# Kernel optimization log

Measured on AMD Instinct MI355X. Metric: run time of the kernel, lower is better.

The kernel has to match this reference:

```python
import jax, jax.numpy as jnp
import numpy as np

N_NODES = 100000
N_EDGES = 1000000
N_GRAPHS = 512
IN_DIM = 3
HID = 64


def setup_inputs() -> dict:
    key = jax.random.key(0)
    ks = jax.random.split(key, 7)
    x = jax.random.normal(ks[0], (N_NODES, IN_DIM), dtype=jnp.float32)
    edge_index = jax.random.randint(ks[1], (2, N_EDGES), 0, N_NODES, dtype=jnp.int64)
    batch = jnp.sort(jax.random.randint(ks[2], (N_NODES,), 0, N_GRAPHS, dtype=jnp.int64))
    # Glorot-ish init for GCNConv linear weights (PyG uses glorot), zero bias.
    W1 = jax.random.normal(ks[3], (IN_DIM, HID), dtype=jnp.float32) / np.float32(np.sqrt(IN_DIM))
    b1 = jnp.zeros((HID,), dtype=jnp.float32)
    W2 = jax.random.normal(ks[4], (HID, HID), dtype=jnp.float32) / np.float32(np.sqrt(HID))
    b2 = jnp.zeros((HID,), dtype=jnp.float32)
    return {"x": x, "W1": W1, "b1": b1, "W2": W2, "b2": b2,
            "edge_index": edge_index, "batch": batch}


def reference(x, W1, b1, W2, b2, edge_index, batch):
    n = x.shape[0]
    loop = jnp.arange(n)
    # GCNConv adds self-loops, then symmetric normalization D^-1/2 (A+I) D^-1/2
    src = jnp.concatenate([edge_index[0], loop])  # [E+N]
    dst = jnp.concatenate([edge_index[1], loop])  # [E+N]
    deg = jax.ops.segment_sum(jnp.ones(dst.shape[0], x.dtype), dst, num_segments=n)
    dinv = jnp.where(deg > 0, jax.lax.rsqrt(deg), 0.0)
    norm = dinv[src] * dinv[dst]  # [E+N]

    def gcn_conv(h, W, b):
        hw = h @ W                       # [N, out] linear first (PyG order)
        msg = hw[src] * norm[:, None]    # gather + scale, [E+N, out]
        agg = jax.ops.segment_sum(msg, dst, num_segments=n)  # scatter-add
        return agg + b

    h = jax.nn.relu(gcn_conv(x, W1, b1))
    h = jax.nn.relu(gcn_conv(h, W2, b2))

    # global_mean_pool over the batch vector
    sums = jax.ops.segment_sum(h, batch, num_segments=N_GRAPHS)          # [G, HID]
    counts = jax.ops.segment_sum(jnp.ones(n, h.dtype), batch, num_segments=N_GRAPHS)
    return sums / jnp.maximum(counts, 1.0)[:, None]
```

## Files before the change

### kernel.cpp

```cpp
#include <hip/hip_runtime.h>

#define HID 64
#define N_GRAPHS_C 512
#define BSHIFT 8
#define NBUCK_MAX 512
#define CAP 3264
#define EPB 4096

typedef unsigned short u16;
typedef unsigned int u32;
typedef unsigned long long u64;

__device__ __forceinline__ float bf2f(u16 u) {
    union { u32 i; float f; } v; v.i = ((u32)u) << 16; return v.f;
}
__device__ __forceinline__ u16 f2bf(float f) {
    union { float f; u32 i; } v; v.f = f;
    u32 x = v.i;
    return (u16)((x + 0x7fffu + ((x >> 16) & 1u)) >> 16);
}


__global__ void bin_pairs(const int* __restrict__ src, const int* __restrict__ dst,
                          int* __restrict__ gcursor, u32* __restrict__ pairs,
                          int nE, int nbuck) {
    __shared__ int lh[NBUCK_MAX];
    __shared__ int lbase[NBUCK_MAX];
    int t = threadIdx.x;
    lh[t] = 0; lh[t + 256] = 0;
    __syncthreads();
    int base = blockIdx.x * EPB;
    u32 pk[16]; int rj[16], bj[16];
    #pragma unroll
    for (int j = 0; j < 16; ++j) {
        int e = base + j * 256 + t;
        if (e < nE) {
            int s = src[e], d = dst[e];
            bj[j] = d >> BSHIFT;
            pk[j] = ((u32)(d & 255) << 17) | (u32)s;
            rj[j] = atomicAdd(&lh[bj[j]], 1);
        } else {
            bj[j] = -1;
        }
    }
    __syncthreads();
    for (int b = t; b < nbuck; b += 256)
        lbase[b] = (lh[b] > 0) ? atomicAdd(&gcursor[b], lh[b]) : 0;
    __syncthreads();
    #pragma unroll
    for (int j = 0; j < 16; ++j) {
        if (bj[j] >= 0) {
            int pos = bj[j] * CAP + lbase[bj[j]] + rj[j];
            pairs[pos] = pk[j];
        }
    }
}

__global__ void build_csr(const u32* __restrict__ pairs, const int* __restrict__ gcursor,
                          int* __restrict__ csr_src, int2* __restrict__ off2,
                          float* __restrict__ dinv, const float* __restrict__ x,
                          float4* __restrict__ xs, u16* __restrict__ A16, int n) {
    __shared__ int hist[256];
    __shared__ int tmp[256];
    int t = threadIdx.x;
    int b = blockIdx.x;
    int pbeg = b * CAP;
    int pend = pbeg + gcursor[b];
    hist[t] = 0;
    if (b == 0 && t < 32) ((u32*)(A16 + (size_t)n * HID))[t] = 0;
    __syncthreads();
    for (int i = pbeg + t; i < pend; i += 256)
        atomicAdd(&hist[pairs[i] >> 17], 1);
    __syncthreads();
    int v = hist[t];
    tmp[t] = v;
    __syncthreads();
    for (int d = 1; d < 256; d <<= 1) {
        int add = (t >= d) ? tmp[t - d] : 0;
        __syncthreads();
        tmp[t] += add;
        __syncthreads();
    }
    int e = pbeg + tmp[t] - v;
    int node = (b << BSHIFT) + t;
    if (node < n) {
        float dv = rsqrtf((float)(v + 1));
        off2[node] = make_int2(e, e + v);
        dinv[node] = dv;
        xs[node] = make_float4(x[3*node]*dv, x[3*node+1]*dv, x[3*node+2]*dv, dv);
    }
    hist[t] = e;
    __syncthreads();
    for (int i = pbeg + t; i < pend; i += 256) {
        u32 p = pairs[i];
        int pos = atomicAdd(&hist[p >> 17], 1);
        csr_src[pos] = (int)(p & 0x1FFFFu);
    }
}


__global__ void agg3(const float4* __restrict__ xs, const int* __restrict__ csr_src,
                     const int2* __restrict__ off2, float4* __restrict__ agg4, int n) {
    int node = blockIdx.x * blockDim.x + threadIdx.x;
    if (node >= n) return;
    int2 be = off2[node];
    int beg = be.x, end = be.y;
    float4 self = xs[node];
    float a0 = 0.f, a1 = 0.f, a2 = 0.f;
    for (int k = beg; k < end; k += 8) {
        int e1 = end - 1;
        int idx[8];
        float4 v[8];
        #pragma unroll
        for (int j = 0; j < 8; ++j) idx[j] = csr_src[min(k + j, e1)];
        #pragma unroll
        for (int j = 0; j < 8; ++j) v[j] = xs[idx[j]];
        #pragma unroll
        for (int j = 0; j < 8; ++j) {
            if (k + j < end) { a0 += v[j].x; a1 += v[j].y; a2 += v[j].z; }
        }
    }
    agg4[node] = make_float4(a0 + self.x, a1 + self.y, a2 + self.z, self.w);
}


#define MM2_NODES 32
__global__ void mm2f(const float4* __restrict__ agg4, const float* __restrict__ W1,
                     const float* __restrict__ b1, const float* __restrict__ W2,
                     u16* __restrict__ A16, int n) {
    __shared__ float w[HID * HID];
    __shared__ float h[MM2_NODES * HID];
    __shared__ float dd[MM2_NODES];
    int t = threadIdx.x;
    for (int i = t; i < HID * HID; i += 256) w[i] = W2[i];
    int base = blockIdx.x * MM2_NODES;
    for (int i = t; i < MM2_NODES * HID; i += 256) {
        int node = base + (i >> 6);
        int f = i & 63;
        float hv = 0.0f;
        if (node < n) {
            float4 a = agg4[node];
            float v = (a.x * W1[f] + a.y * W1[HID + f] + a.z * W1[2 * HID + f]) * a.w + b1[f];
            hv = v > 0.0f ? v : 0.0f;
            if (f == 0) dd[i >> 6] = a.w;
        }
        h[i] = hv;
    }
    __syncthreads();
    int f = t & 63, g = t >> 6;
    float acc[8];
    #pragma unroll
    for (int j = 0; j < 8; ++j) acc[j] = 0.0f;
    #pragma unroll 4
    for (int k = 0; k < HID; ++k) {
        float wk = w[k * HID + f];
        #pragma unroll
        for (int j = 0; j < 8; ++j) acc[j] += h[(g * 8 + j) * HID + k] * wk;
    }
    #pragma unroll
    for (int j = 0; j < 8; ++j) {
        int node = base + g * 8 + j;
        if (node < n) A16[(size_t)node * HID + f] = f2bf(acc[j] * dd[g * 8 + j]);
    }
}


__global__ void gather_nodes(const u16* __restrict__ A16, const float* __restrict__ dinv,
                             const int* __restrict__ csr_src, const int2* __restrict__ off2,
                             const float* __restrict__ bias,
                             u16* __restrict__ H16, int n) {
    int t = threadIdx.x;
    int waveq = t >> 4;
    int m = t & 15;
    int qbase = t & 48;
    int node = blockIdx.x * 16 + waveq;
    if (node >= n) return;
    int2 be = off2[node];
    int beg = be.x, end = be.y;
    u64 selfrow = *(const u64*)(A16 + ((size_t)node << 6) + (m << 2));
    u32 slo = (u32)selfrow, shi = (u32)(selfrow >> 32);
    float acc0 = bf2f((u16)(slo & 0xffffu));
    float acc1 = bf2f((u16)(slo >> 16));
    float acc2 = bf2f((u16)(shi & 0xffffu));
    float acc3 = bf2f((u16)(shi >> 16));
    const char* Ab = (const char*)A16;
    u32 laneoff = (u32)(m << 3);
    for (int k = beg; k < end; k += 16) {
        int nIdx = end - k;
        int myIdx = (m < nIdx) ? csr_src[k + m] : n;
        #pragma unroll
        for (int j0 = 0; j0 < 16; j0 += 8) {
            int ss[8]; u64 rows[8];
            #pragma unroll
            for (int j = 0; j < 8; ++j)
                ss[j] = __shfl(myIdx, qbase + j0 + j, 64);
            #pragma unroll
            for (int j = 0; j < 8; ++j)
                rows[j] = *(const u64*)(Ab + (((u32)ss[j] << 7) | laneoff));
            #pragma unroll
            for (int j = 0; j < 8; ++j) {
                u32 lo = (u32)rows[j], hi = (u32)(rows[j] >> 32);
                acc0 += bf2f((u16)(lo & 0xffffu));
                acc1 += bf2f((u16)(lo >> 16));
                acc2 += bf2f((u16)(hi & 0xffffu));
                acc3 += bf2f((u16)(hi >> 16));
            }
        }
    }
    float ddv = dinv[node];
    float4 bb = *(const float4*)(bias + (m << 2));
    float v0 = fmaxf(acc0 * ddv + bb.x, 0.0f);
    float v1 = fmaxf(acc1 * ddv + bb.y, 0.0f);
    float v2 = fmaxf(acc2 * ddv + bb.z, 0.0f);
    float v3 = fmaxf(acc3 * ddv + bb.w, 0.0f);
    u64 outp = (u64)f2bf(v0) | ((u64)f2bf(v1) << 16)
             | ((u64)f2bf(v2) << 32) | ((u64)f2bf(v3) << 48);
    *(u64*)(H16 + ((size_t)node << 6) + (m << 2)) = outp;
}


__device__ __forceinline__ int lower_bound(const int* __restrict__ a, int n, int key) {
    int lo = 0, hi = n;
    while (lo < hi) {
        int mid = (lo + hi) >> 1;
        if (a[mid] < key) lo = mid + 1; else hi = mid;
    }
    return lo;
}

__global__ void graph_ranges(const int* __restrict__ batch, int* __restrict__ gstart,
                             int n, int nGraphs) {
    for (int g = threadIdx.x; g <= nGraphs; g += blockDim.x)
        gstart[g] = lower_bound(batch, n, g);
}


__global__ void pool_graph(const u16* __restrict__ H16, const int* __restrict__ gstart,
                           float* __restrict__ out, int n) {
    int g = blockIdx.x;
    int t = threadIdx.x;
    int lo = gstart[g];
    int hi = gstart[g + 1];
    int cntN = hi - lo;
    int sid = t >> 4;
    int m = t & 15;
    float a0 = 0.f, a1 = 0.f, a2 = 0.f, a3 = 0.f;
    int i = lo + sid;
    for (; i + 16 < hi; i += 32) {
        u64 r0 = *(const u64*)(H16 + ((size_t)i << 6) + (m << 2));
        u64 r1 = *(const u64*)(H16 + ((size_t)(i + 16) << 6) + (m << 2));
        u32 l0 = (u32)r0, h0 = (u32)(r0 >> 32);
        u32 l1 = (u32)r1, h1 = (u32)(r1 >> 32);
        a0 += bf2f((u16)(l0 & 0xffffu)) + bf2f((u16)(l1 & 0xffffu));
        a1 += bf2f((u16)(l0 >> 16))     + bf2f((u16)(l1 >> 16));
        a2 += bf2f((u16)(h0 & 0xffffu)) + bf2f((u16)(h1 & 0xffffu));
        a3 += bf2f((u16)(h0 >> 16))     + bf2f((u16)(h1 >> 16));
    }
    if (i < hi) {
        u64 r0 = *(const u64*)(H16 + ((size_t)i << 6) + (m << 2));
        u32 l0 = (u32)r0, h0 = (u32)(r0 >> 32);
        a0 += bf2f((u16)(l0 & 0xffffu));
        a1 += bf2f((u16)(l0 >> 16));
        a2 += bf2f((u16)(h0 & 0xffffu));
        a3 += bf2f((u16)(h0 >> 16));
    }
    a0 += __shfl_xor(a0, 16, 64); a0 += __shfl_xor(a0, 32, 64);
    a1 += __shfl_xor(a1, 16, 64); a1 += __shfl_xor(a1, 32, 64);
    a2 += __shfl_xor(a2, 16, 64); a2 += __shfl_xor(a2, 32, 64);
    a3 += __shfl_xor(a3, 16, 64); a3 += __shfl_xor(a3, 32, 64);
    __shared__ float smf[4 * HID];
    int wave = t >> 6, lane = t & 63;
    if (lane < 16) {
        smf[wave * HID + 4 * lane + 0] = a0;
        smf[wave * HID + 4 * lane + 1] = a1;
        smf[wave * HID + 4 * lane + 2] = a2;
        smf[wave * HID + 4 * lane + 3] = a3;
    }
    __syncthreads();
    if (t < HID) {
        float s = smf[t] + smf[HID + t] + smf[2 * HID + t] + smf[3 * HID + t];
        out[(size_t)g * HID + t] = s / fmaxf((float)cntN, 1.0f);
    }
}


extern "C" void kernel_launch(void* const* d_in, const int* in_sizes, int n_in,
                              void* d_out, int out_size, void* d_ws, size_t ws_size,
                              hipStream_t stream) {
    const float* x  = (const float*)d_in[0];
    const float* W1 = (const float*)d_in[1];
    const float* b1 = (const float*)d_in[2];
    const float* W2 = (const float*)d_in[3];
    const float* b2 = (const float*)d_in[4];
    const int*   ei = (const int*)d_in[5];
    const int*   batch = (const int*)d_in[6];

    const int n  = in_sizes[0] / 3;
    const int nE = in_sizes[5] / 2;
    const int* src = ei;
    const int* dst = ei + nE;
    const int nbuck = (n + ((1 << BSHIFT) - 1)) >> BSHIFT;
    const int nGraphs = out_size / HID;

    char* p = (char*)d_ws;
    int*    gcursor = (int*)p;                p += 2048;
    int*    gstart  = (int*)p;                p += 4096;
    int*    csr_src = (int*)p;                p += (size_t)nbuck * CAP * 4;
    int2*   off2    = (int2*)p;               p += (size_t)n * 8;
    float*  dinv    = (float*)p;              p += (size_t)n * 4;
    float4* xs      = (float4*)p;             p += (size_t)n * 16;
    float4* agg4    = (float4*)p;             p += (size_t)n * 16;
    u16*    A16     = (u16*)p;                p += (size_t)(n + 1) * HID * 2;
    u16*    H2      = (u16*)p;                p += (size_t)n * HID * 2;
    u32*    pairs   = (u32*)A16;

    const int BT = 256;
    const int gridNode = (n + BT - 1) / BT;
    const int gridE2   = (nE + EPB - 1) / EPB;
    const int gridMM2  = (n + MM2_NODES - 1) / MM2_NODES;
    const int gridGath = (n + 15) / 16;

    hipMemsetAsync(gcursor, 0, 2048, stream);
    bin_pairs<<<gridE2, BT, 0, stream>>>(src, dst, gcursor, pairs, nE, nbuck);
    build_csr<<<nbuck, BT, 0, stream>>>(pairs, gcursor, csr_src, off2, dinv, x, xs, A16, n);

    graph_ranges<<<1, 512, 0, stream>>>(batch, gstart, n, nGraphs);

    agg3<<<gridNode, BT, 0, stream>>>(xs, csr_src, off2, agg4, n);
    mm2f<<<gridMM2, BT, 0, stream>>>(agg4, W1, b1, W2, A16, n);

    gather_nodes<<<gridGath, BT, 0, stream>>>(A16, dinv, csr_src, off2, b2, H2, n);

    pool_graph<<<nGraphs, BT, 0, stream>>>(H2, gstart, (float*)d_out, n);
}
```

Before: 172.0 us.

## Fuse memset with graph-range prep, widen binning blocks, shrink gather unroll

Replaces the memset and the graph_ranges launch with a single prep kernel that zeroes the bucket cursors and computes graph start offsets, removing one launch and one memset. bin_pairs and build_csr now run with 512 threads per block, so bin_pairs keeps 8 edges per thread instead of 16 and build_csr guards its 256-wide scan and node work to the first 256 threads. The second-layer gather loop handles 8 neighbours per iteration instead of 16, which wastes fewer padded lanes on low-degree nodes but leaves fewer loads in flight per iteration. The zeroing in prep relies on nbuck being at most 512.

```diff
diff --git a/kernel.cpp b/kernel.cpp
--- a/kernel.cpp
+++ b/kernel.cpp
@@ -21,19 +21,37 @@
 }
 
 
+__device__ __forceinline__ int lower_bound(const int* __restrict__ a, int n, int key) {
+    int lo = 0, hi = n;
+    while (lo < hi) {
+        int mid = (lo + hi) >> 1;
+        if (a[mid] < key) lo = mid + 1; else hi = mid;
+    }
+    return lo;
+}
+
+__global__ void prep(int* __restrict__ gcursor, const int* __restrict__ batch,
+                     int* __restrict__ gstart, int n, int nGraphs) {
+    int t = threadIdx.x;
+    gcursor[t] = 0;
+    for (int g = t; g <= nGraphs; g += 512)
+        gstart[g] = lower_bound(batch, n, g);
+}
+
+
 __global__ void bin_pairs(const int* __restrict__ src, const int* __restrict__ dst,
                           int* __restrict__ gcursor, u32* __restrict__ pairs,
                           int nE, int nbuck) {
     __shared__ int lh[NBUCK_MAX];
     __shared__ int lbase[NBUCK_MAX];
     int t = threadIdx.x;
-    lh[t] = 0; lh[t + 256] = 0;
+    lh[t] = 0;
     __syncthreads();
     int base = blockIdx.x * EPB;
-    u32 pk[16]; int rj[16], bj[16];
+    u32 pk[8]; int rj[8], bj[8];
     #pragma unroll
-    for (int j = 0; j < 16; ++j) {
-        int e = base + j * 256 + t;
+    for (int j = 0; j < 8; ++j) {
+        int e = base + j * 512 + t;
         if (e < nE) {
             int s = src[e], d = dst[e];
             bj[j] = d >> BSHIFT;
@@ -44,11 +62,10 @@
         }
     }
     __syncthreads();
-    for (int b = t; b < nbuck; b += 256)
-        lbase[b] = (lh[b] > 0) ? atomicAdd(&gcursor[b], lh[b]) : 0;
+    if (t < nbuck) lbase[t] = (lh[t] > 0) ? atomicAdd(&gcursor[t], lh[t]) : 0;
     __syncthreads();
     #pragma unroll
-    for (int j = 0; j < 16; ++j) {
+    for (int j = 0; j < 8; ++j) {
         if (bj[j] >= 0) {
             int pos = bj[j] * CAP + lbase[bj[j]] + rj[j];
             pairs[pos] = pk[j];
@@ -66,32 +83,34 @@
     int b = blockIdx.x;
     int pbeg = b * CAP;
     int pend = pbeg + gcursor[b];
-    hist[t] = 0;
+    if (t < 256) hist[t] = 0;
     if (b == 0 && t < 32) ((u32*)(A16 + (size_t)n * HID))[t] = 0;
     __syncthreads();
-    for (int i = pbeg + t; i < pend; i += 256)
+    for (int i = pbeg + t; i < pend; i += 512)
         atomicAdd(&hist[pairs[i] >> 17], 1);
     __syncthreads();
-    int v = hist[t];
-    tmp[t] = v;
+    int v = 0;
+    if (t < 256) { v = hist[t]; tmp[t] = v; }
     __syncthreads();
     for (int d = 1; d < 256; d <<= 1) {
-        int add = (t >= d) ? tmp[t - d] : 0;
+        int add = (t >= d && t < 256) ? tmp[t - d] : 0;
         __syncthreads();
-        tmp[t] += add;
+        if (t < 256) tmp[t] += add;
         __syncthreads();
     }
-    int e = pbeg + tmp[t] - v;
-    int node = (b << BSHIFT) + t;
-    if (node < n) {
-        float dv = rsqrtf((float)(v + 1));
-        off2[node] = make_int2(e, e + v);
-        dinv[node] = dv;
-        xs[node] = make_float4(x[3*node]*dv, x[3*node+1]*dv, x[3*node+2]*dv, dv);
-    }
-    hist[t] = e;
-    __syncthreads();
-    for (int i = pbeg + t; i < pend; i += 256) {
+    if (t < 256) {
+        int e = pbeg + tmp[t] - v;
+        int node = (b << BSHIFT) + t;
+        if (node < n) {
+            float dv = rsqrtf((float)(v + 1));
+            off2[node] = make_int2(e, e + v);
+            dinv[node] = dv;
+            xs[node] = make_float4(x[3*node]*dv, x[3*node+1]*dv, x[3*node+2]*dv, dv);
+        }
+        hist[t] = e;
+    }
+    __syncthreads();
+    for (int i = pbeg + t; i < pend; i += 512) {
         u32 p = pairs[i];
         int pos = atomicAdd(&hist[p >> 17], 1);
         csr_src[pos] = (int)(p & 0x1FFFFu);
@@ -185,26 +204,23 @@
     float acc3 = bf2f((u16)(shi >> 16));
     const char* Ab = (const char*)A16;
     u32 laneoff = (u32)(m << 3);
-    for (int k = beg; k < end; k += 16) {
-        int nIdx = end - k;
-        int myIdx = (m < nIdx) ? csr_src[k + m] : n;
-        #pragma unroll
-        for (int j0 = 0; j0 < 16; j0 += 8) {
-            int ss[8]; u64 rows[8];
-            #pragma unroll
-            for (int j = 0; j < 8; ++j)
-                ss[j] = __shfl(myIdx, qbase + j0 + j, 64);
-            #pragma unroll
-            for (int j = 0; j < 8; ++j)
-                rows[j] = *(const u64*)(Ab + (((u32)ss[j] << 7) | laneoff));
-            #pragma unroll
-            for (int j = 0; j < 8; ++j) {
-                u32 lo = (u32)rows[j], hi = (u32)(rows[j] >> 32);
-                acc0 += bf2f((u16)(lo & 0xffffu));
-                acc1 += bf2f((u16)(lo >> 16));
-                acc2 += bf2f((u16)(hi & 0xffffu));
-                acc3 += bf2f((u16)(hi >> 16));
-            }
+    for (int k = beg; k < end; k += 8) {
+        int lim = min(end - k, 8);
+        int myIdx = (m < lim) ? csr_src[k + m] : n;
+        int ss[8]; u64 rows[8];
+        #pragma unroll
+        for (int j = 0; j < 8; ++j)
+            ss[j] = __shfl(myIdx, qbase + j, 64);
+        #pragma unroll
+        for (int j = 0; j < 8; ++j)
+            rows[j] = *(const u64*)(Ab + (((u32)ss[j] << 7) | laneoff));
+        #pragma unroll
+        for (int j = 0; j < 8; ++j) {
+            u32 lo = (u32)rows[j], hi = (u32)(rows[j] >> 32);
+            acc0 += bf2f((u16)(lo & 0xffffu));
+            acc1 += bf2f((u16)(lo >> 16));
+            acc2 += bf2f((u16)(hi & 0xffffu));
+            acc3 += bf2f((u16)(hi >> 16));
         }
     }
     float ddv = dinv[node];
@@ -216,22 +232,6 @@
     u64 outp = (u64)f2bf(v0) | ((u64)f2bf(v1) << 16)
              | ((u64)f2bf(v2) << 32) | ((u64)f2bf(v3) << 48);
     *(u64*)(H16 + ((size_t)node << 6) + (m << 2)) = outp;
-}
-
-
-__device__ __forceinline__ int lower_bound(const int* __restrict__ a, int n, int key) {
-    int lo = 0, hi = n;
-    while (lo < hi) {
-        int mid = (lo + hi) >> 1;
-        if (a[mid] < key) lo = mid + 1; else hi = mid;
-    }
-    return lo;
-}
-
-__global__ void graph_ranges(const int* __restrict__ batch, int* __restrict__ gstart,
-                             int n, int nGraphs) {
-    for (int g = threadIdx.x; g <= nGraphs; g += blockDim.x)
-        gstart[g] = lower_bound(batch, n, g);
 }
 
 
@@ -320,11 +320,9 @@
     const int gridMM2  = (n + MM2_NODES - 1) / MM2_NODES;
     const int gridGath = (n + 15) / 16;
 
-    hipMemsetAsync(gcursor, 0, 2048, stream);
-    bin_pairs<<<gridE2, BT, 0, stream>>>(src, dst, gcursor, pairs, nE, nbuck);
-    build_csr<<<nbuck, BT, 0, stream>>>(pairs, gcursor, csr_src, off2, dinv, x, xs, A16, n);
-
-    graph_ranges<<<1, 512, 0, stream>>>(batch, gstart, n, nGraphs);
+    prep<<<1, 512, 0, stream>>>(gcursor, batch, gstart, n, nGraphs);
+    bin_pairs<<<gridE2, 512, 0, stream>>>(src, dst, gcursor, pairs, nE, nbuck);
+    build_csr<<<nbuck, 512, 0, stream>>>(pairs, gcursor, csr_src, off2, dinv, x, xs, A16, n);
 
     agg3<<<gridNode, BT, 0, stream>>>(xs, csr_src, off2, agg4, n);
     mm2f<<<gridMM2, BT, 0, stream>>>(agg4, W1, b1, W2, A16, n);
```

Result: no change. 168.9 us (-1.8%).
